# Kernel tuning notes

Hardware: AMD Instinct MI355X
Metric: run time of the kernel (lower is better)

Reference implementation:

```python
import jax, jax.numpy as jnp
import numpy as np

EPS = 1e-8
NUM_ITERS = 3
STDEV = 0.1  # dense layer weight init scale (applied in setup)


def squash(s, axis=-1):
    # squash(s) = (|s|^2 / (1 + |s|^2)) * s / |s|
    n2 = jnp.sum(s * s, axis=axis, keepdims=True)
    return s * (n2 / (1.0 + n2)) / jnp.sqrt(n2 + EPS)


def setup_inputs() -> dict:
    key = jax.random.key(0)
    k1, k2 = jax.random.split(key)
    b, i, j, n_in, n_out = 32, 2048, 64, 16, 32
    x = jax.random.normal(k1, (b, i, n_in), dtype=jnp.float32)
    W = STDEV * jax.random.normal(k2, (j, i, n_out, n_in), dtype=jnp.float32)
    bias = jnp.zeros((j, n_out), dtype=jnp.float32)
    return {"x": x, "W": W, "bias": bias}


def reference(x, W, bias):
    # Dense capsule layer: u_hat[b,j,i,m] = sum_n W[j,i,m,n] * x[b,i,n]
    u_hat = jnp.einsum("bin,jimn->bjim", x, W)  # [b, j, i, n_out]
    b_, j_, i_, _ = u_hat.shape

    logits = jnp.zeros((b_, j_, i_), dtype=u_hat.dtype)
    v = None
    for it in range(NUM_ITERS):
        c = jax.nn.softmax(logits, axis=1)  # softmax over parent capsules j
        # weighted sum over children i, plus routing bias
        s = jnp.einsum("bji,bjim->bjm", c, u_hat) + bias  # [b, j, n_out]
        v = squash(s)  # [b, j, n_out]
        if it < NUM_ITERS - 1:
            # agreement: <v_j, u_hat_{j,i}>
            logits = logits + jnp.einsum("bjm,bjim->bji", v, u_hat)
    return v
```

## Files before the change

kernel.cpp:

```cpp
#include <hip/hip_runtime.h>

constexpr float FEPS = 1e-8f;

typedef __attribute__((ext_vector_type(8)))  short bf16x8;
typedef __attribute__((ext_vector_type(16))) float f32x16;

__device__ __forceinline__ short bf16_rne(float f) {
    unsigned u = __float_as_uint(f);
    return (short)((u + 0x7FFFu + ((u >> 16) & 1u)) >> 16);
}
__device__ __forceinline__ float bf16_val(short h) {
    return __uint_as_float(((unsigned)(unsigned short)h) << 16);
}
__device__ __forceinline__ void cvt8(float4 a, float4 b, bf16x8& hi, bf16x8& lo) {
    float v[8] = {a.x, a.y, a.z, a.w, b.x, b.y, b.z, b.w};
    #pragma unroll
    for (int e = 0; e < 8; ++e) {
        const short hb = bf16_rne(v[e]);
        hi[e] = hb;
        lo[e] = bf16_rne(v[e] - bf16_val(hb));
    }
}
#define MFMA(A, B, C) __builtin_amdgcn_mfma_f32_32x32x16_bf16((A), (B), (C), 0, 0, 0)

__global__ __launch_bounds__(512, 2)
void stats_pass(const float* __restrict__ W, const float* __restrict__ x,
                const float* __restrict__ veff, float* __restrict__ Zinv)
{
    __shared__ float zred[8][32][5];
    const int tid = threadIdx.x;
    const int l = tid & 63, w = tid >> 6;
    const int b = l & 31, h = l >> 5;
    const int i0 = blockIdx.x * 4;

    bf16x8 xh[4], xl[4];
    #pragma unroll
    for (int ii = 0; ii < 4; ++ii) {
        const float* xr = x + (((size_t)b << 15) + ((size_t)(i0 + ii) << 4) + (h << 3));
        cvt8(*(const float4*)xr, *(const float4*)(xr + 4), xh[ii], xl[ii]);
    }
    float zacc[4] = {0.f, 0.f, 0.f, 0.f};

    #pragma unroll 1
    for (int jt = 0; jt < 8; ++jt) {
        const int j = w + (jt << 3);
        const float* vr = veff + ((((size_t)b << 6) | (size_t)j) << 5) + (h << 2);
        const float4 vq0 = *(const float4*)(vr + 0);
        const float4 vq1 = *(const float4*)(vr + 8);
        const float4 vq2 = *(const float4*)(vr + 16);
        const float4 vq3 = *(const float4*)(vr + 24);
        const float* wrow = W + (((size_t)j << 20) + ((size_t)i0 << 9) + (b << 4) + (h << 3));
        #pragma unroll
        for (int ii = 0; ii < 4; ++ii) {
            bf16x8 wh, wl;
            cvt8(*(const float4*)wrow, *(const float4*)(wrow + 4), wh, wl);
            wrow += 512;
            f32x16 u;
            #pragma unroll
            for (int r = 0; r < 16; ++r) u[r] = 0.f;
            u = MFMA(wh, xh[ii], u);
            u = MFMA(wh, xl[ii], u);
            u = MFMA(wl, xh[ii], u);
            float th = 0.f;
            th = fmaf(u[0],  vq0.x, th); th = fmaf(u[1],  vq0.y, th);
            th = fmaf(u[2],  vq0.z, th); th = fmaf(u[3],  vq0.w, th);
            th = fmaf(u[4],  vq1.x, th); th = fmaf(u[5],  vq1.y, th);
            th = fmaf(u[6],  vq1.z, th); th = fmaf(u[7],  vq1.w, th);
            th = fmaf(u[8],  vq2.x, th); th = fmaf(u[9],  vq2.y, th);
            th = fmaf(u[10], vq2.z, th); th = fmaf(u[11], vq2.w, th);
            th = fmaf(u[12], vq3.x, th); th = fmaf(u[13], vq3.y, th);
            th = fmaf(u[14], vq3.z, th); th = fmaf(u[15], vq3.w, th);
            const float t = th + __shfl_xor(th, 32, 64);
            zacc[ii] += __expf(t);
        }
    }
    if (h == 0) {
        #pragma unroll
        for (int ii = 0; ii < 4; ++ii) zred[w][b][ii] = zacc[ii];
    }
    __syncthreads();
    if (tid < 128) {
        const int bb = tid >> 2, ii = tid & 3;
        float z = 0.f;
        #pragma unroll
        for (int ww = 0; ww < 8; ++ww) z += zred[ww][bb][ii];
        Zinv[((size_t)bb << 11) + i0 + ii] = 1.0f / z;
    }
}

template<int MODE>
__global__ __launch_bounds__(512, 2)
void accum_pass(const float* __restrict__ W, const float* __restrict__ x,
                const float* __restrict__ veff, const float* __restrict__ Zinv,
                float* __restrict__ sbuf)
{
    __shared__ float sred[8][32][36];
    const int tid = threadIdx.x;
    const int l = tid & 63, w = tid >> 6;
    const int b = l & 31, h = l >> 5;
    const int j  = blockIdx.x >> 3;
    const int iq = blockIdx.x & 7;
    const int ibase = iq * 256 + w * 32;

    float4 vq0, vq1, vq2, vq3;
    if (MODE) {
        const float* vr = veff + ((((size_t)b << 6) | (size_t)j) << 5) + (h << 2);
        vq0 = *(const float4*)(vr + 0);
        vq1 = *(const float4*)(vr + 8);
        vq2 = *(const float4*)(vr + 16);
        vq3 = *(const float4*)(vr + 24);
    }
    f32x16 accs;
    #pragma unroll
    for (int r = 0; r < 16; ++r) accs[r] = 0.f;

    const float* wrow = W + (((size_t)j << 20) + ((size_t)ibase << 9) + (b << 4) + (h << 3));
    #pragma unroll 2
    for (int ii = 0; ii < 32; ++ii) {
        const int i = ibase + ii;
        const float* xr = x + (((size_t)b << 15) + ((size_t)i << 4) + (h << 3));
        bf16x8 xh, xl, wh, wl;
        cvt8(*(const float4*)xr, *(const float4*)(xr + 4), xh, xl);
        cvt8(*(const float4*)wrow, *(const float4*)(wrow + 4), wh, wl);
        wrow += 512;
        if (MODE == 0) {
            accs = MFMA(wh, xh, accs);
            accs = MFMA(wh, xl, accs);
            accs = MFMA(wl, xh, accs);
        } else {
            f32x16 u;
            #pragma unroll
            for (int r = 0; r < 16; ++r) u[r] = 0.f;
            u = MFMA(wh, xh, u);
            u = MFMA(wh, xl, u);
            u = MFMA(wl, xh, u);
            float th = 0.f;
            th = fmaf(u[0],  vq0.x, th); th = fmaf(u[1],  vq0.y, th);
            th = fmaf(u[2],  vq0.z, th); th = fmaf(u[3],  vq0.w, th);
            th = fmaf(u[4],  vq1.x, th); th = fmaf(u[5],  vq1.y, th);
            th = fmaf(u[6],  vq1.z, th); th = fmaf(u[7],  vq1.w, th);
            th = fmaf(u[8],  vq2.x, th); th = fmaf(u[9],  vq2.y, th);
            th = fmaf(u[10], vq2.z, th); th = fmaf(u[11], vq2.w, th);
            th = fmaf(u[12], vq3.x, th); th = fmaf(u[13], vq3.y, th);
            th = fmaf(u[14], vq3.z, th); th = fmaf(u[15], vq3.w, th);
            const float t = th + __shfl_xor(th, 32, 64);
            const float c = __expf(t) * Zinv[((size_t)b << 11) + i];
            #pragma unroll
            for (int r = 0; r < 16; ++r) accs[r] = fmaf(c, u[r], accs[r]);
        }
    }
    const float scale = (MODE == 0) ? 0.015625f : 1.0f;
    #pragma unroll
    for (int q = 0; q < 4; ++q) {
        *(float4*)&sred[w][b][q * 8 + (h << 2)] =
            make_float4(accs[q*4] * scale, accs[q*4+1] * scale,
                        accs[q*4+2] * scale, accs[q*4+3] * scale);
    }
    __syncthreads();
    #pragma unroll
    for (int k = 0; k < 2; ++k) {
        const int idx = tid * 2 + k;
        const int bb = idx >> 5, mm = idx & 31;
        float s = 0.f;
        #pragma unroll
        for (int ww = 0; ww < 8; ++ww) s += sred[ww][bb][mm];
        atomicAdd(sbuf + ((((size_t)bb << 6) | (size_t)j) << 5) + mm, s);
    }
}

__global__ __launch_bounds__(256)
void squash_pass(float* __restrict__ sbuf, const float* __restrict__ bias,
                 float* __restrict__ vout, const float* __restrict__ vold)
{
    const int tid = threadIdx.x;
    const int m = tid & 31, g = tid >> 5;
    const int pair = blockIdx.x * 8 + g;
    const int j = pair & 63;
    const size_t idx = ((size_t)pair << 5) + m;
    float s = sbuf[idx] + bias[(j << 5) + m];
    sbuf[idx] = 0.f;
    float n2 = s * s;
    n2 += __shfl_xor(n2, 1, 64);  n2 += __shfl_xor(n2, 2, 64);
    n2 += __shfl_xor(n2, 4, 64);  n2 += __shfl_xor(n2, 8, 64);
    n2 += __shfl_xor(n2, 16, 64);
    float v = s * (n2 / (1.f + n2)) / sqrtf(n2 + FEPS);
    if (vold) v += vold[idx];
    vout[idx] = v;
}

extern "C" void kernel_launch(void* const* d_in, const int* in_sizes, int n_in,
                              void* d_out, int out_size, void* d_ws, size_t ws_size,
                              hipStream_t stream)
{
    const float* x    = (const float*)d_in[0];
    const float* W    = (const float*)d_in[1];
    const float* bias = (const float*)d_in[2];
    float* out  = (float*)d_out;
    float* sbuf = (float*)d_ws;
    float* Zinv = sbuf + 65536;

    hipMemsetAsync(sbuf, 0, 65536 * sizeof(float), stream);

    accum_pass<0><<<512, 512, 0, stream>>>(W, x, nullptr, nullptr, sbuf);
    squash_pass<<<256, 256, 0, stream>>>(sbuf, bias, out, nullptr);
    stats_pass<<<512, 512, 0, stream>>>(W, x, out, Zinv);
    accum_pass<1><<<512, 512, 0, stream>>>(W, x, out, Zinv, sbuf);
    squash_pass<<<256, 256, 0, stream>>>(sbuf, bias, out, out);
    stats_pass<<<512, 512, 0, stream>>>(W, x, out, Zinv);
    accum_pass<1><<<512, 512, 0, stream>>>(W, x, out, Zinv, sbuf);
    squash_pass<<<256, 256, 0, stream>>>(sbuf, bias, out, nullptr);
}
```

Baseline: 310.0 us.

## Use single bf16 MFMA in stats pass and fuse squash into accumulate via last-block

```diff
diff --git a/kernel.cpp b/kernel.cpp
--- a/kernel.cpp
+++ b/kernel.cpp
@@ -12,7 +12,7 @@
 __device__ __forceinline__ float bf16_val(short h) {
     return __uint_as_float(((unsigned)(unsigned short)h) << 16);
 }
-__device__ __forceinline__ void cvt8(float4 a, float4 b, bf16x8& hi, bf16x8& lo) {
+__device__ __forceinline__ void cvt8(const float4 a, const float4 b, bf16x8& hi, bf16x8& lo) {
     float v[8] = {a.x, a.y, a.z, a.w, b.x, b.y, b.z, b.w};
     #pragma unroll
     for (int e = 0; e < 8; ++e) {
@@ -20,6 +20,13 @@
         hi[e] = hb;
         lo[e] = bf16_rne(v[e] - bf16_val(hb));
     }
+}
+__device__ __forceinline__ bf16x8 cvt8hi(const float4 a, const float4 b) {
+    float v[8] = {a.x, a.y, a.z, a.w, b.x, b.y, b.z, b.w};
+    bf16x8 hi;
+    #pragma unroll
+    for (int e = 0; e < 8; ++e) hi[e] = bf16_rne(v[e]);
+    return hi;
 }
 #define MFMA(A, B, C) __builtin_amdgcn_mfma_f32_32x32x16_bf16((A), (B), (C), 0, 0, 0)
 
@@ -33,11 +40,11 @@
     const int b = l & 31, h = l >> 5;
     const int i0 = blockIdx.x * 4;
 
-    bf16x8 xh[4], xl[4];
+    bf16x8 xh[4];
     #pragma unroll
     for (int ii = 0; ii < 4; ++ii) {
         const float* xr = x + (((size_t)b << 15) + ((size_t)(i0 + ii) << 4) + (h << 3));
-        cvt8(*(const float4*)xr, *(const float4*)(xr + 4), xh[ii], xl[ii]);
+        xh[ii] = cvt8hi(*(const float4*)xr, *(const float4*)(xr + 4));
     }
     float zacc[4] = {0.f, 0.f, 0.f, 0.f};
 
@@ -52,15 +59,12 @@
         const float* wrow = W + (((size_t)j << 20) + ((size_t)i0 << 9) + (b << 4) + (h << 3));
         #pragma unroll
         for (int ii = 0; ii < 4; ++ii) {
-            bf16x8 wh, wl;
-            cvt8(*(const float4*)wrow, *(const float4*)(wrow + 4), wh, wl);
+            const bf16x8 wh = cvt8hi(*(const float4*)wrow, *(const float4*)(wrow + 4));
             wrow += 512;
             f32x16 u;
             #pragma unroll
             for (int r = 0; r < 16; ++r) u[r] = 0.f;
             u = MFMA(wh, xh[ii], u);
-            u = MFMA(wh, xl[ii], u);
-            u = MFMA(wl, xh[ii], u);
             float th = 0.f;
             th = fmaf(u[0],  vq0.x, th); th = fmaf(u[1],  vq0.y, th);
             th = fmaf(u[2],  vq0.z, th); th = fmaf(u[3],  vq0.w, th);
@@ -88,13 +92,16 @@
     }
 }
 
-template<int MODE>
+template<int MODE, bool ADDOLD>
 __global__ __launch_bounds__(512, 2)
 void accum_pass(const float* __restrict__ W, const float* __restrict__ x,
                 const float* __restrict__ veff, const float* __restrict__ Zinv,
-                float* __restrict__ sbuf)
+                float* __restrict__ sbuf, const float* __restrict__ bias,
+                float* __restrict__ vout, const float* __restrict__ vold,
+                int* __restrict__ counter)
 {
     __shared__ float sred[8][32][36];
+    __shared__ int lastFlag;
     const int tid = threadIdx.x;
     const int l = tid & 63, w = tid >> 6;
     const int b = l & 31, h = l >> 5;
@@ -166,26 +173,29 @@
         for (int ww = 0; ww < 8; ++ww) s += sred[ww][bb][mm];
         atomicAdd(sbuf + ((((size_t)bb << 6) | (size_t)j) << 5) + mm, s);
     }
-}
-
-__global__ __launch_bounds__(256)
-void squash_pass(float* __restrict__ sbuf, const float* __restrict__ bias,
-                 float* __restrict__ vout, const float* __restrict__ vold)
-{
-    const int tid = threadIdx.x;
+
+    __threadfence();
+    if (tid == 0)
+        lastFlag = (atomicAdd(counter, 1) == (int)gridDim.x - 1);
+    __syncthreads();
+    if (!lastFlag) return;
+    __threadfence();
     const int m = tid & 31, g = tid >> 5;
-    const int pair = blockIdx.x * 8 + g;
-    const int j = pair & 63;
-    const size_t idx = ((size_t)pair << 5) + m;
-    float s = sbuf[idx] + bias[(j << 5) + m];
-    sbuf[idx] = 0.f;
-    float n2 = s * s;
-    n2 += __shfl_xor(n2, 1, 64);  n2 += __shfl_xor(n2, 2, 64);
-    n2 += __shfl_xor(n2, 4, 64);  n2 += __shfl_xor(n2, 8, 64);
-    n2 += __shfl_xor(n2, 16, 64);
-    float v = s * (n2 / (1.f + n2)) / sqrtf(n2 + FEPS);
-    if (vold) v += vold[idx];
-    vout[idx] = v;
+    for (int pair = g; pair < 2048; pair += 16) {
+        const int jj = pair & 63;
+        const size_t idx = ((size_t)pair << 5) + m;
+        float s = __hip_atomic_load(&sbuf[idx], __ATOMIC_RELAXED, __HIP_MEMORY_SCOPE_AGENT)
+                + bias[(jj << 5) + m];
+        sbuf[idx] = 0.f;
+        float n2 = s * s;
+        n2 += __shfl_xor(n2, 1, 64);  n2 += __shfl_xor(n2, 2, 64);
+        n2 += __shfl_xor(n2, 4, 64);  n2 += __shfl_xor(n2, 8, 64);
+        n2 += __shfl_xor(n2, 16, 64);
+        float v = s * (n2 / (1.f + n2)) / sqrtf(n2 + FEPS);
+        if (ADDOLD) v += vold[idx];
+        vout[idx] = v;
+    }
+    if (tid == 0) *counter = 0;
 }
 
 extern "C" void kernel_launch(void* const* d_in, const int* in_sizes, int n_in,
@@ -198,15 +208,13 @@
     float* out  = (float*)d_out;
     float* sbuf = (float*)d_ws;
     float* Zinv = sbuf + 65536;
-
-    hipMemsetAsync(sbuf, 0, 65536 * sizeof(float), stream);
-
-    accum_pass<0><<<512, 512, 0, stream>>>(W, x, nullptr, nullptr, sbuf);
-    squash_pass<<<256, 256, 0, stream>>>(sbuf, bias, out, nullptr);
+    int*   ctr  = (int*)(sbuf + 131072);
+
+    hipMemsetAsync(d_ws, 0, 131073 * sizeof(float), stream);
+
+    accum_pass<0, false><<<512, 512, 0, stream>>>(W, x, nullptr, nullptr, sbuf, bias, out, nullptr, ctr);
     stats_pass<<<512, 512, 0, stream>>>(W, x, out, Zinv);
-    accum_pass<1><<<512, 512, 0, stream>>>(W, x, out, Zinv, sbuf);
-    squash_pass<<<256, 256, 0, stream>>>(sbuf, bias, out, out);
+    accum_pass<1, true ><<<512, 512, 0, stream>>>(W, x, out, Zinv, sbuf, bias, out, out, ctr);
     stats_pass<<<512, 512, 0, stream>>>(W, x, out, Zinv);
-    accum_pass<1><<<512, 512, 0, stream>>>(W, x, out, Zinv, sbuf);
-    squash_pass<<<256, 256, 0, stream>>>(sbuf, bias, out, nullptr);
-}
+    accum_pass<1, false><<<512, 512, 0, stream>>>(W, x, out, Zinv, sbuf, bias, out, nullptr, ctr);
+}
```

Measured after the change: 1.127 ms. 3.64x slower.
